# Optimization experiments

Measured on AMD Instinct MI355X. Metric: run time of the kernel, lower is better.

## Reference

```python
import jax, jax.numpy as jnp
import numpy as np

HEADS = 8
DIM_HEAD = 64
QUERY_DIM = 256
CONTEXT_DIM = 512
HIDDEN = HEADS * DIM_HEAD  # 512


def setup_inputs() -> dict:
    key = jax.random.key(0)
    ks = jax.random.split(key, 7)
    x = jax.random.normal(ks[0], (4, QUERY_DIM, 64, 64), dtype=jnp.float32)
    context = jax.random.normal(ks[1], (4, CONTEXT_DIM, 32, 32), dtype=jnp.float32)
    # 1x1 conv weights stored as [out_ch, in_ch]
    Wq = jax.random.normal(ks[2], (HIDDEN, QUERY_DIM), dtype=jnp.float32) * (QUERY_DIM ** -0.5)
    Wk = jax.random.normal(ks[3], (HIDDEN, CONTEXT_DIM), dtype=jnp.float32) * (CONTEXT_DIM ** -0.5)
    Wv = jax.random.normal(ks[4], (HIDDEN, CONTEXT_DIM), dtype=jnp.float32) * (CONTEXT_DIM ** -0.5)
    Wo = jax.random.normal(ks[5], (QUERY_DIM, HIDDEN), dtype=jnp.float32) * (HIDDEN ** -0.5)
    bo = jax.random.normal(ks[6], (QUERY_DIM,), dtype=jnp.float32) * 0.01
    return {"x": x, "context": context, "Wq": Wq, "Wk": Wk, "Wv": Wv, "Wo": Wo, "bo": bo}


def reference(x, context, Wq, Wk, Wv, Wo, bo):
    b, c, h, w = x.shape
    _, _, hc, wc = context.shape
    scale = DIM_HEAD ** -0.5
    # 1x1 convs == channel matmuls
    q = jnp.einsum('oc,bchw->bohw', Wq, x).reshape(b, HEADS, DIM_HEAD, h * w)
    k = jnp.einsum('oc,bchw->bohw', Wk, context).reshape(b, HEADS, DIM_HEAD, hc * wc)
    v = jnp.einsum('oc,bchw->bohw', Wv, context).reshape(b, HEADS, DIM_HEAD, hc * wc)
    sim = jnp.einsum('bhci,bhcj->bhij', q, k) * scale  # [b,H,h*w,hc*wc]
    attn = jax.nn.softmax(sim, axis=-1)
    out = jnp.einsum('bhij,bhcj->bhci', attn, v)  # [b,H,dim_head,h*w]
    out = out.reshape(b, HIDDEN, h, w)
    return jnp.einsum('oc,bchw->bohw', Wo, out) + bo[None, :, None, None]
```

## Files before the change

### kernel.cpp

```cpp
#include <hip/hip_runtime.h>
#include <math.h>
#include <stdint.h>

#define BATCH 4
#define CQ 256
#define P 4096
#define CC 512
#define PC 1024
#define HID 512
#define HEADS 8
#define DH 64

#define QSCALE 0.180336880111113703f

typedef __attribute__((ext_vector_type(8))) __fp16 f16x8;
typedef __attribute__((ext_vector_type(2))) __fp16 f16x2;
typedef __attribute__((ext_vector_type(4))) float f32x4;
typedef __attribute__((ext_vector_type(4))) unsigned int u32x4;

union H2U { f16x2 h; uint32_t u; };
union F8U { uint32_t u[4]; f16x8 v; };

__device__ __forceinline__ uint32_t pkh(float a, float b) {
    H2U z; z.h = __builtin_amdgcn_cvt_pkrtz(a, b); return z.u;
}
__device__ __forceinline__ f16x2 upk(uint32_t w) { H2U z; z.u = w; return z.h; }

#if __has_builtin(__builtin_amdgcn_exp2f)
#define EXP2(x) __builtin_amdgcn_exp2f(x)
#else
#define EXP2(x) exp2f(x)
#endif

#define MFMA16(a, b, c) __builtin_amdgcn_mfma_f32_16x16x32_f16(a, b, c, 0, 0, 0)

__device__ __forceinline__ void gl_lds16(const unsigned short* g, unsigned short* l) {
    __builtin_amdgcn_global_load_lds(
        (const __attribute__((address_space(1))) unsigned int*)g,
        (__attribute__((address_space(3))) unsigned int*)l, 16, 0, 0);
}

__global__ __launch_bounds__(256) void split_all(
    const float* __restrict__ Wq, const float* __restrict__ Wk,
    const float* __restrict__ Wv, const float* __restrict__ Wo,
    unsigned short* __restrict__ wqh, unsigned short* __restrict__ wkh,
    unsigned short* __restrict__ wvh, unsigned short* __restrict__ woh)
{
    const int bid = blockIdx.x;
    const int t = threadIdx.x;
    const float* src; unsigned short* dh; int i4; float sc = 1.f; int ksh;
    if (bid < 128)      { src = Wq; dh = wqh; i4 = bid * 256 + t; sc = QSCALE; ksh = 8; }
    else if (bid < 384) { src = Wk; dh = wkh; i4 = (bid - 128) * 256 + t; ksh = 9; }
    else if (bid < 640) { src = Wv; dh = wvh; i4 = (bid - 384) * 256 + t; ksh = 9; }
    else                { src = Wo; dh = woh; i4 = (bid - 640) * 256 + t; ksh = 0; }
    float4 v = *reinterpret_cast<const float4*>(src + (size_t)i4 * 4);
    uint2 hh;
    hh.x = pkh(sc * v.x, sc * v.y);
    hh.y = pkh(sc * v.z, sc * v.w);
    if (ksh) {
        const int lin = i4 * 4;
        const int m = lin >> ksh;
        const int k = lin & ((1 << ksh) - 1);
        const size_t off = ((size_t)(k >> 3) * HID + m) * 8 + (k & 7);
        *reinterpret_cast<uint2*>(dh + off) = hh;
    } else {
        *reinterpret_cast<uint2*>(dh + (size_t)i4 * 4) = hh;
    }
}

__global__ __launch_bounds__(256) void proj_qkv(
    const unsigned short* __restrict__ wqh_, const unsigned short* __restrict__ wkh_,
    const unsigned short* __restrict__ wvh_,
    const float* __restrict__ x_, const float* __restrict__ ctx_,
    unsigned short* __restrict__ qh_,
    unsigned short* __restrict__ kh_, unsigned short* __restrict__ vh_)
{
    const int b = blockIdx.z;
    const int bx = blockIdx.x;
    const int wid = threadIdx.x >> 6;
    const int l = threadIdx.x & 63;
    const int ln = l & 15, g = l >> 4;
    const int mb = blockIdx.y * 128 + 64 * (wid & 1);

    f32x4 acc[4][2];
    #pragma unroll
    for (int mt = 0; mt < 4; ++mt)
        #pragma unroll
        for (int nt = 0; nt < 2; ++nt) {
            f32x4 z = {0.f, 0.f, 0.f, 0.f};
            acc[mt][nt] = z;
        }

    int mode;
    int nb;
    if (bx < 64) {
        mode = 0;
        nb = bx * 64 + 32 * (wid >> 1);
        const float* xb = x_ + (size_t)b * CQ * P;
        #pragma unroll 2
        for (int k0 = 0; k0 < CQ; k0 += 32) {
            const int kq = (k0 >> 3) + g;
            f16x8 ah[4];
            #pragma unroll
            for (int mt = 0; mt < 4; ++mt)
                ah[mt] = *reinterpret_cast<const f16x8*>(
                    wqh_ + ((size_t)kq * HID + mb + 16 * mt + ln) * 8);
            #pragma unroll
            for (int nt = 0; nt < 2; ++nt) {
                const int pos = nb + 16 * nt + ln;
                float v0 = xb[(size_t)(8 * kq + 0) * P + pos];
                float v1 = xb[(size_t)(8 * kq + 1) * P + pos];
                float v2 = xb[(size_t)(8 * kq + 2) * P + pos];
                float v3 = xb[(size_t)(8 * kq + 3) * P + pos];
                float v4 = xb[(size_t)(8 * kq + 4) * P + pos];
                float v5 = xb[(size_t)(8 * kq + 5) * P + pos];
                float v6 = xb[(size_t)(8 * kq + 6) * P + pos];
                float v7 = xb[(size_t)(8 * kq + 7) * P + pos];
                F8U bh;
                bh.u[0] = pkh(v0, v1); bh.u[1] = pkh(v2, v3);
                bh.u[2] = pkh(v4, v5); bh.u[3] = pkh(v6, v7);
                #pragma unroll
                for (int mt = 0; mt < 4; ++mt)
                    acc[mt][nt] = MFMA16(ah[mt], bh.v, acc[mt][nt]);
            }
        }
    } else {
        const int u = bx - 64;
        mode = 1 + (u >> 4);
        nb = (u & 15) * 64 + 32 * (wid >> 1);
        const unsigned short* Ah = (mode == 2) ? wvh_ : wkh_;
        const float* cb = ctx_ + (size_t)b * CC * PC;
        #pragma unroll 2
        for (int k0 = 0; k0 < CC; k0 += 32) {
            const int kq = (k0 >> 3) + g;
            f16x8 ah[4];
            #pragma unroll
            for (int mt = 0; mt < 4; ++mt)
                ah[mt] = *reinterpret_cast<const f16x8*>(
                    Ah + ((size_t)kq * HID + mb + 16 * mt + ln) * 8);
            #pragma unroll
            for (int nt = 0; nt < 2; ++nt) {
                const int pos = nb + 16 * nt + ln;
                float v0 = cb[(size_t)(8 * kq + 0) * PC + pos];
                float v1 = cb[(size_t)(8 * kq + 1) * PC + pos];
                float v2 = cb[(size_t)(8 * kq + 2) * PC + pos];
                float v3 = cb[(size_t)(8 * kq + 3) * PC + pos];
                float v4 = cb[(size_t)(8 * kq + 4) * PC + pos];
                float v5 = cb[(size_t)(8 * kq + 5) * PC + pos];
                float v6 = cb[(size_t)(8 * kq + 6) * PC + pos];
                float v7 = cb[(size_t)(8 * kq + 7) * PC + pos];
                F8U bh;
                bh.u[0] = pkh(v0, v1); bh.u[1] = pkh(v2, v3);
                bh.u[2] = pkh(v4, v5); bh.u[3] = pkh(v6, v7);
                #pragma unroll
                for (int mt = 0; mt < 4; ++mt)
                    acc[mt][nt] = MFMA16(ah[mt], bh.v, acc[mt][nt]);
            }
        }
    }

    if (mode == 0) {
        #pragma unroll
        for (int mt = 0; mt < 4; ++mt) {
            const int m0 = mb + 16 * mt + 4 * g;
            const int h = m0 >> 6, cl2 = m0 & 63;
            #pragma unroll
            for (int nt = 0; nt < 2; ++nt) {
                const int pos = nb + 16 * nt + ln;
                uint2 hh;
                hh.x = pkh(acc[mt][nt][0], acc[mt][nt][1]);
                hh.y = pkh(acc[mt][nt][2], acc[mt][nt][3]);
                const size_t base = (((size_t)b * HEADS + h) * P + pos) * 64 + cl2;
                *reinterpret_cast<uint2*>(qh_ + base) = hh;
            }
        }
    } else if (mode == 1) {
        #pragma unroll
        for (int mt = 0; mt < 4; ++mt) {
            const int m0 = mb + 16 * mt + 4 * g;
            const int h = m0 >> 6, cl2 = m0 & 63;
            #pragma unroll
            for (int nt = 0; nt < 2; ++nt) {
                const int pos = nb + 16 * nt + ln;
                uint2 hh;
                hh.x = pkh(acc[mt][nt][0], acc[mt][nt][1]);
                hh.y = pkh(acc[mt][nt][2], acc[mt][nt][3]);
                const size_t base = (((size_t)b * HEADS + h) * PC + pos) * 64 + cl2;
                *reinterpret_cast<uint2*>(kh_ + base) = hh;
            }
        }
    } else {
        #pragma unroll
        for (int mt = 0; mt < 4; ++mt) {
            const int m0 = mb + 16 * mt + 4 * g;
            #pragma unroll
            for (int nt = 0; nt < 2; ++nt) {
                const int pos = nb + 16 * nt + ln;
                #pragma unroll
                for (int r = 0; r < 4; ++r) {
                    unsigned short hv =
                        (unsigned short)(pkh(acc[mt][nt][r], 0.f) & 0xffffu);
                    vh_[((size_t)b * HID + m0 + r) * PC + pos] = hv;
                }
            }
        }
    }
}

#define NIN 4
#define JBLK 64
#define NJT (PC / JBLK)

__global__ __launch_bounds__(256, 2) void attn_mfma(
    const unsigned short* __restrict__ qh,
    const unsigned short* __restrict__ kh,
    const unsigned short* __restrict__ vh,
    uint32_t* __restrict__ oh)
{
    const int wid = threadIdx.x >> 6;
    const int l = threadIdx.x & 63;
    const int ln = l & 15, g = l >> 4;
    const int rx = ln & 7;
    const int hb = blockIdx.x;
    const int h = hb & 7, b = hb >> 3;
    const int i0 = (blockIdx.y * 4 + wid) * 64;

    const size_t qbase = (size_t)(b * HEADS + h) * P * 64;
    const size_t kbase = (size_t)(b * HEADS + h) * PC * 64;
    const size_t vbase = (size_t)(b * HID + h * DH) * PC;

    __shared__ unsigned short smem[2][8192];

    f16x8 qf[NIN][2];
    #pragma unroll
    for (int in_ = 0; in_ < NIN; ++in_) {
        const size_t qrow = qbase + (size_t)(i0 + 16 * in_ + ln) * 64 + 8 * g;
        #pragma unroll
        for (int ks = 0; ks < 2; ++ks)
            qf[in_][ks] = *reinterpret_cast<const f16x8*>(qh + qrow + 32 * ks);
    }

    f32x4 acc[4][NIN];
    #pragma unroll
    for (int cm = 0; cm < 4; ++cm)
        #pragma unroll
        for (int in_ = 0; in_ < NIN; ++in_) {
            f32x4 z = {0.f, 0.f, 0.f, 0.f};
            acc[cm][in_] = z;
        }
    float lsum[NIN];
    #pragma unroll
    for (int in_ = 0; in_ < NIN; ++in_) lsum[in_] = 0.f;

    const int idx0 = ln + 16 * (2 * (g & 1));
    const int idx1 = idx0 + 16;
    const bool topTile = (g & 2) != 0;

    auto stage = [&](int buf, int jt) {
        const int j0 = jt * JBLK;
        #pragma unroll
        for (int t = 0; t < 4; ++t) {
            const int s = wid * 4 + t;
            unsigned short* lbase = &smem[buf][s * 512];
            const int e = (s & 7) * 64 + l;
            const int row = e >> 3, p = e & 7;
            const int slog = p ^ (row & 7);
            const unsigned short* src;
            if (s < 8) {
                src = kh + kbase + (size_t)(j0 + row) * 64 + 8 * slog;
            } else {
                src = vh + vbase + (size_t)row * PC + j0 + 8 * slog;
            }
            gl_lds16(src, lbase);
        }
    };

    stage(0, 0);
    __syncthreads();

    for (int jt = 0; jt < NJT; ++jt) {
        const int cur = jt & 1;
        if (jt + 1 < NJT) stage(cur ^ 1, jt + 1);
        const unsigned short* sm = &smem[cur][0];

        #pragma unroll 1
        for (int half = 0; half < 2; ++half) {
            f16x8 kf[2][2];
            #pragma unroll
            for (int jm = 0; jm < 2; ++jm)
                #pragma unroll
                for (int ks = 0; ks < 2; ++ks) {
                    const int base = (32 * half + 16 * jm + ln) * 64 +
                                     8 * ((4 * ks + g) ^ rx);
                    kf[jm][ks] = *reinterpret_cast<const f16x8*>(sm + base);
                }
            f16x8 vf[4];
            #pragma unroll
            for (int cm = 0; cm < 4; ++cm) {
                const int vaddr = 4096 + (16 * cm + ln) * 64 +
                                  8 * ((4 * half + g) ^ rx);
                vf[cm] = *reinterpret_cast<const f16x8*>(sm + vaddr);
            }

            f32x4 s[2][NIN];
            #pragma unroll
            for (int jm = 0; jm < 2; ++jm)
                #pragma unroll
                for (int in_ = 0; in_ < NIN; ++in_) {
                    f32x4 z = {0.f, 0.f, 0.f, 0.f};
                    s[jm][in_] = z;
                }
            __builtin_amdgcn_s_setprio(1);
            #pragma unroll
            for (int jm = 0; jm < 2; ++jm)
                #pragma unroll
                for (int ks = 0; ks < 2; ++ks)
                    #pragma unroll
                    for (int in_ = 0; in_ < NIN; ++in_)
                        s[jm][in_] = MFMA16(kf[jm][ks], qf[in_][ks], s[jm][in_]);
            __builtin_amdgcn_s_setprio(0);

            #pragma unroll
            for (int in_ = 0; in_ < NIN; ++in_) {
                float ls = 0.f;
                #pragma unroll
                for (int jm = 0; jm < 2; ++jm)
                    #pragma unroll
                    for (int r = 0; r < 4; ++r) {
                        float p = EXP2(s[jm][in_][r]);
                        s[jm][in_][r] = p; ls += p;
                    }
                lsum[in_] += ls;

                int w00 = (int)pkh(s[0][in_][0], s[0][in_][1]);
                int w01 = (int)pkh(s[0][in_][2], s[0][in_][3]);
                int w10 = (int)pkh(s[1][in_][0], s[1][in_][1]);
                int w11 = (int)pkh(s[1][in_][2], s[1][in_][3]);

                int a0 = __shfl(w00, idx0, 64), a1 = __shfl(w01, idx0, 64);
                int a2 = __shfl(w00, idx1, 64), a3 = __shfl(w01, idx1, 64);
                int b0 = __shfl(w10, idx0, 64), b1 = __shfl(w11, idx0, 64);
                int b2 = __shfl(w10, idx1, 64), b3 = __shfl(w11, idx1, 64);
                F8U fu;
                fu.u[0] = (uint32_t)(topTile ? b0 : a0);
                fu.u[1] = (uint32_t)(topTile ? b1 : a1);
                fu.u[2] = (uint32_t)(topTile ? b2 : a2);
                fu.u[3] = (uint32_t)(topTile ? b3 : a3);

                __builtin_amdgcn_s_setprio(1);
                #pragma unroll
                for (int cm = 0; cm < 4; ++cm)
                    acc[cm][in_] = MFMA16(vf[cm], fu.v, acc[cm][in_]);
                __builtin_amdgcn_s_setprio(0);
            }
        }

        __syncthreads();
    }

    #pragma unroll
    for (int in_ = 0; in_ < NIN; ++in_) {
        float lt = lsum[in_];
        lt += __shfl_xor(lt, 16, 64);
        lt += __shfl_xor(lt, 32, 64);
        float inv = 1.0f / lt;
        int i = i0 + 16 * in_ + ln;
        #pragma unroll
        for (int cm = 0; cm < 4; ++cm) {
            f32x4 o4 = acc[cm][in_] * inv;
            const int cp = 32 * h + 8 * cm + 2 * g;
            const size_t idx = ((size_t)b * 256 + cp) * P + i;
            oh[idx] = pkh(o4[0], o4[1]);
            oh[idx + P] = pkh(o4[2], o4[3]);
        }
    }
}

__global__ __launch_bounds__(256, 4) void out_proj(
    const unsigned short* __restrict__ woh, const uint32_t* __restrict__ oh,
    const float* __restrict__ bo, float* __restrict__ out)
{
    const int wid = threadIdx.x >> 6;
    const int l = threadIdx.x & 63;
    const int ln = l & 15, g = l >> 4;
    const int ibase = blockIdx.x * 128 + wid * 32;
    const int otile = blockIdx.y * 32;
    const int b = blockIdx.z;

    f32x4 acc[2][2];
    #pragma unroll
    for (int mt = 0; mt < 2; ++mt)
        #pragma unroll
        for (int nt = 0; nt < 2; ++nt) {
            f32x4 z = {0.f, 0.f, 0.f, 0.f};
            acc[mt][nt] = z;
        }

    #pragma unroll
    for (int ks = 0; ks < 16; ++ks) {
        const int c0 = 32 * ks + 8 * g;
        const int cp0 = c0 >> 1;
        f16x8 wf[2];
        #pragma unroll
        for (int mt = 0; mt < 2; ++mt)
            wf[mt] = *reinterpret_cast<const f16x8*>(
                woh + (size_t)(otile + 16 * mt + ln) * HID + c0);
        #pragma unroll
        for (int nt = 0; nt < 2; ++nt) {
            const int pos = ibase + 16 * nt + ln;
            const size_t obase = ((size_t)b * 256 + cp0) * P + pos;
            F8U bh;
            bh.u[0] = oh[obase];
            bh.u[1] = oh[obase + P];
            bh.u[2] = oh[obase + 2 * (size_t)P];
            bh.u[3] = oh[obase + 3 * (size_t)P];
            #pragma unroll
            for (int mt = 0; mt < 2; ++mt)
                acc[mt][nt] = MFMA16(wf[mt], bh.v, acc[mt][nt]);
        }
    }

    #pragma unroll
    for (int mt = 0; mt < 2; ++mt)
        #pragma unroll
        for (int r = 0; r < 4; ++r) {
            int o_ = otile + 16 * mt + 4 * g + r;
            float bv = bo[o_];
            #pragma unroll
            for (int nt = 0; nt < 2; ++nt)
                out[((size_t)b * CQ + o_) * P + ibase + 16 * nt + ln] =
                    acc[mt][nt][r] + bv;
        }
}

extern "C" void kernel_launch(void* const* d_in, const int* in_sizes, int n_in,
                              void* d_out, int out_size, void* d_ws, size_t ws_size,
                              hipStream_t stream) {
    (void)in_sizes; (void)n_in; (void)out_size; (void)ws_size;
    const float* x   = (const float*)d_in[0];
    const float* ctx = (const float*)d_in[1];
    const float* Wq  = (const float*)d_in[2];
    const float* Wk  = (const float*)d_in[3];
    const float* Wv  = (const float*)d_in[4];
    const float* Wo  = (const float*)d_in[5];
    const float* bo  = (const float*)d_in[6];
    float* out = (float*)d_out;

    unsigned short* ws = (unsigned short*)d_ws;
    uint32_t* oh        = (uint32_t*)ws;
    unsigned short* qh  = ws + (size_t)8388608;
    unsigned short* kh  = qh + (size_t)8388608;
    unsigned short* vh  = kh + (size_t)2097152;
    unsigned short* woh = vh + (size_t)2097152;
    unsigned short* wqh = woh + (size_t)131072;
    unsigned short* wkh = wqh + (size_t)131072;
    unsigned short* wvh = wkh + (size_t)262144;

    dim3 blk(256);
    split_all<<<dim3(768), blk, 0, stream>>>(Wq, Wk, Wv, Wo, wqh, wkh, wvh, woh);
    proj_qkv<<<dim3(96, 4, BATCH), blk, 0, stream>>>(
        wqh, wkh, wvh, x, ctx, qh, kh, vh);
    attn_mfma<<<dim3(HEADS * BATCH, P / 256), blk, 0, stream>>>(
        qh, kh, vh, oh);
    out_proj<<<dim3(P / 128, CQ / 32, BATCH), blk, 0, stream>>>(
        woh, oh, bo, out);
}
```

Before: 113.8 us.

## Widen QKV projection M-tile and transpose softmax probabilities through LDS

The QKV projection now gives each wave 128 output channels instead of 64 and halves the grid's y dimension. Each converted input fragment is reused across twice as many MFMAs, which halves the redundant fp32 activation loads and fp16 conversions. The cost is more accumulator registers; launch bounds ask for 2 blocks per CU. In the attention kernel, the eight cross-lane shuffles plus selects that re-lay out the P fragments become a small per-wave LDS write and 128-bit read, trading shuffle traffic for LDS traffic with no barrier.

```diff
diff --git a/kernel.cpp b/kernel.cpp
--- a/kernel.cpp
+++ b/kernel.cpp
@@ -68,7 +68,7 @@
     }
 }
 
-__global__ __launch_bounds__(256) void proj_qkv(
+__global__ __launch_bounds__(256, 2) void proj_qkv(
     const unsigned short* __restrict__ wqh_, const unsigned short* __restrict__ wkh_,
     const unsigned short* __restrict__ wvh_,
     const float* __restrict__ x_, const float* __restrict__ ctx_,
@@ -80,11 +80,11 @@
     const int wid = threadIdx.x >> 6;
     const int l = threadIdx.x & 63;
     const int ln = l & 15, g = l >> 4;
-    const int mb = blockIdx.y * 128 + 64 * (wid & 1);
-
-    f32x4 acc[4][2];
-    #pragma unroll
-    for (int mt = 0; mt < 4; ++mt)
+    const int mb = blockIdx.y * 256 + 128 * (wid & 1);
+
+    f32x4 acc[8][2];
+    #pragma unroll
+    for (int mt = 0; mt < 8; ++mt)
         #pragma unroll
         for (int nt = 0; nt < 2; ++nt) {
             f32x4 z = {0.f, 0.f, 0.f, 0.f};
@@ -100,11 +100,7 @@
         #pragma unroll 2
         for (int k0 = 0; k0 < CQ; k0 += 32) {
             const int kq = (k0 >> 3) + g;
-            f16x8 ah[4];
-            #pragma unroll
-            for (int mt = 0; mt < 4; ++mt)
-                ah[mt] = *reinterpret_cast<const f16x8*>(
-                    wqh_ + ((size_t)kq * HID + mb + 16 * mt + ln) * 8);
+            F8U bh[2];
             #pragma unroll
             for (int nt = 0; nt < 2; ++nt) {
                 const int pos = nb + 16 * nt + ln;
@@ -116,12 +112,15 @@
                 float v5 = xb[(size_t)(8 * kq + 5) * P + pos];
                 float v6 = xb[(size_t)(8 * kq + 6) * P + pos];
                 float v7 = xb[(size_t)(8 * kq + 7) * P + pos];
-                F8U bh;
-                bh.u[0] = pkh(v0, v1); bh.u[1] = pkh(v2, v3);
-                bh.u[2] = pkh(v4, v5); bh.u[3] = pkh(v6, v7);
-                #pragma unroll
-                for (int mt = 0; mt < 4; ++mt)
-                    acc[mt][nt] = MFMA16(ah[mt], bh.v, acc[mt][nt]);
+                bh[nt].u[0] = pkh(v0, v1); bh[nt].u[1] = pkh(v2, v3);
+                bh[nt].u[2] = pkh(v4, v5); bh[nt].u[3] = pkh(v6, v7);
+            }
+            #pragma unroll
+            for (int mt = 0; mt < 8; ++mt) {
+                f16x8 ah = *reinterpret_cast<const f16x8*>(
+                    wqh_ + ((size_t)kq * HID + mb + 16 * mt + ln) * 8);
+                acc[mt][0] = MFMA16(ah, bh[0].v, acc[mt][0]);
+                acc[mt][1] = MFMA16(ah, bh[1].v, acc[mt][1]);
             }
         }
     } else {
@@ -133,11 +132,7 @@
         #pragma unroll 2
         for (int k0 = 0; k0 < CC; k0 += 32) {
             const int kq = (k0 >> 3) + g;
-            f16x8 ah[4];
-            #pragma unroll
-            for (int mt = 0; mt < 4; ++mt)
-                ah[mt] = *reinterpret_cast<const f16x8*>(
-                    Ah + ((size_t)kq * HID + mb + 16 * mt + ln) * 8);
+            F8U bh[2];
             #pragma unroll
             for (int nt = 0; nt < 2; ++nt) {
                 const int pos = nb + 16 * nt + ln;
@@ -149,19 +144,22 @@
                 float v5 = cb[(size_t)(8 * kq + 5) * PC + pos];
                 float v6 = cb[(size_t)(8 * kq + 6) * PC + pos];
                 float v7 = cb[(size_t)(8 * kq + 7) * PC + pos];
-                F8U bh;
-                bh.u[0] = pkh(v0, v1); bh.u[1] = pkh(v2, v3);
-                bh.u[2] = pkh(v4, v5); bh.u[3] = pkh(v6, v7);
-                #pragma unroll
-                for (int mt = 0; mt < 4; ++mt)
-                    acc[mt][nt] = MFMA16(ah[mt], bh.v, acc[mt][nt]);
+                bh[nt].u[0] = pkh(v0, v1); bh[nt].u[1] = pkh(v2, v3);
+                bh[nt].u[2] = pkh(v4, v5); bh[nt].u[3] = pkh(v6, v7);
+            }
+            #pragma unroll
+            for (int mt = 0; mt < 8; ++mt) {
+                f16x8 ah = *reinterpret_cast<const f16x8*>(
+                    Ah + ((size_t)kq * HID + mb + 16 * mt + ln) * 8);
+                acc[mt][0] = MFMA16(ah, bh[0].v, acc[mt][0]);
+                acc[mt][1] = MFMA16(ah, bh[1].v, acc[mt][1]);
             }
         }
     }
 
     if (mode == 0) {
         #pragma unroll
-        for (int mt = 0; mt < 4; ++mt) {
+        for (int mt = 0; mt < 8; ++mt) {
             const int m0 = mb + 16 * mt + 4 * g;
             const int h = m0 >> 6, cl2 = m0 & 63;
             #pragma unroll
@@ -176,7 +174,7 @@
         }
     } else if (mode == 1) {
         #pragma unroll
-        for (int mt = 0; mt < 4; ++mt) {
+        for (int mt = 0; mt < 8; ++mt) {
             const int m0 = mb + 16 * mt + 4 * g;
             const int h = m0 >> 6, cl2 = m0 & 63;
             #pragma unroll
@@ -191,7 +189,7 @@
         }
     } else {
         #pragma unroll
-        for (int mt = 0; mt < 4; ++mt) {
+        for (int mt = 0; mt < 8; ++mt) {
             const int m0 = mb + 16 * mt + 4 * g;
             #pragma unroll
             for (int nt = 0; nt < 2; ++nt) {
@@ -230,6 +228,7 @@
     const size_t vbase = (size_t)(b * HID + h * DH) * PC;
 
     __shared__ unsigned short smem[2][8192];
+    __shared__ uint32_t pT[4][16][20];
 
     f16x8 qf[NIN][2];
     #pragma unroll
@@ -251,10 +250,6 @@
     float lsum[NIN];
     #pragma unroll
     for (int in_ = 0; in_ < NIN; ++in_) lsum[in_] = 0.f;
-
-    const int idx0 = ln + 16 * (2 * (g & 1));
-    const int idx1 = idx0 + 16;
-    const bool topTile = (g & 2) != 0;
 
     auto stage = [&](int buf, int jt) {
         const int j0 = jt * JBLK;
@@ -332,20 +327,20 @@
                     }
                 lsum[in_] += ls;
 
-                int w00 = (int)pkh(s[0][in_][0], s[0][in_][1]);
-                int w01 = (int)pkh(s[0][in_][2], s[0][in_][3]);
-                int w10 = (int)pkh(s[1][in_][0], s[1][in_][1]);
-                int w11 = (int)pkh(s[1][in_][2], s[1][in_][3]);
-
-                int a0 = __shfl(w00, idx0, 64), a1 = __shfl(w01, idx0, 64);
-                int a2 = __shfl(w00, idx1, 64), a3 = __shfl(w01, idx1, 64);
-                int b0 = __shfl(w10, idx0, 64), b1 = __shfl(w11, idx0, 64);
-                int b2 = __shfl(w10, idx1, 64), b3 = __shfl(w11, idx1, 64);
+                uint32_t w00 = pkh(s[0][in_][0], s[0][in_][1]);
+                uint32_t w01 = pkh(s[0][in_][2], s[0][in_][3]);
+                uint32_t w10 = pkh(s[1][in_][0], s[1][in_][1]);
+                uint32_t w11 = pkh(s[1][in_][2], s[1][in_][3]);
+
+                uint32_t* pw = &pT[wid][ln][0];
+                uint2 wlo; wlo.x = w00; wlo.y = w01;
+                uint2 whi; whi.x = w10; whi.y = w11;
+                *reinterpret_cast<uint2*>(pw + 2 * g) = wlo;
+                *reinterpret_cast<uint2*>(pw + 8 + 2 * g) = whi;
                 F8U fu;
-                fu.u[0] = (uint32_t)(topTile ? b0 : a0);
-                fu.u[1] = (uint32_t)(topTile ? b1 : a1);
-                fu.u[2] = (uint32_t)(topTile ? b2 : a2);
-                fu.u[3] = (uint32_t)(topTile ? b3 : a3);
+                u32x4 f4 = *reinterpret_cast<const u32x4*>(&pT[wid][ln][4 * g]);
+                fu.u[0] = f4[0]; fu.u[1] = f4[1];
+                fu.u[2] = f4[2]; fu.u[3] = f4[3];
 
                 __builtin_amdgcn_s_setprio(1);
                 #pragma unroll
@@ -458,7 +453,7 @@
 
     dim3 blk(256);
     split_all<<<dim3(768), blk, 0, stream>>>(Wq, Wk, Wv, Wo, wqh, wkh, wvh, woh);
-    proj_qkv<<<dim3(96, 4, BATCH), blk, 0, stream>>>(
+    proj_qkv<<<dim3(96, 2, BATCH), blk, 0, stream>>>(
         wqh, wkh, wvh, x, ctx, qh, kh, vh);
     attn_mfma<<<dim3(HEADS * BATCH, P / 256), blk, 0, stream>>>(
         qh, kh, vh, oh);
```

New measurement: 138.9 us. 1.22x slower.
